# Kernel tuning notes

Measured on AMD Instinct MI355X. Metric: run time of the kernel, lower is better.

## Reference

```python
import jax, jax.numpy as jnp
import numpy as np

N_AGENTS = 5
RNN = 128
ATT = 64
N_ACT = 10
IN_DIM = 256
SIZE = 65535  # multiple of N_AGENTS -> padding branch never taken
TAU = 0.01


def _gru_cell(x, h, w_ih, w_hh, b_ih, b_hh):
    # PyTorch GRUCell math
    gi = x @ w_ih.T + b_ih
    gh = h @ w_hh.T + b_hh
    i_r, i_z, i_n = jnp.split(gi, 3, axis=-1)
    h_r, h_z, h_n = jnp.split(gh, 3, axis=-1)
    r = jax.nn.sigmoid(i_r + h_r)
    z = jax.nn.sigmoid(i_z + h_z)
    n = jnp.tanh(i_n + r * h_n)
    return (1.0 - z) * n + z * h


def _gru_seq(xs, w_ih, w_hh, b_ih, b_hh):
    # xs: [T, B, D]; zero initial hidden, returns all step outputs [T, B, RNN]
    h0 = jnp.zeros((xs.shape[1], RNN), xs.dtype)
    def step(h, x):
        h2 = _gru_cell(x, h, w_ih, w_hh, b_ih, b_hh)
        return h2, h2
    _, ys = jax.lax.scan(step, h0, xs)
    return ys


def setup_inputs():
    key = jax.random.key(0)
    ks = jax.random.split(key, 26)
    def u(k, shape, fan):
        return jax.random.uniform(k, shape, jnp.float32, -1.0, 1.0) / np.sqrt(fan)
    return {
        'obs': jax.random.normal(ks[0], (SIZE, IN_DIM), jnp.float32),
        'hidden_state': jax.random.normal(ks[1], (SIZE, RNN), jnp.float32),
        'enc_w': u(ks[2], (RNN, IN_DIM), IN_DIM), 'enc_b': u(ks[3], (RNN,), IN_DIM),
        'gru_w_ih': u(ks[4], (3 * RNN, RNN), RNN), 'gru_w_hh': u(ks[5], (3 * RNN, RNN), RNN),
        'gru_b_ih': u(ks[6], (3 * RNN,), RNN), 'gru_b_hh': u(ks[7], (3 * RNN,), RNN),
        'bi_w_ih_f': u(ks[8], (3 * RNN, 2 * RNN), RNN), 'bi_w_hh_f': u(ks[9], (3 * RNN, RNN), RNN),
        'bi_b_ih_f': u(ks[10], (3 * RNN,), RNN), 'bi_b_hh_f': u(ks[11], (3 * RNN,), RNN),
        'bi_w_ih_r': u(ks[12], (3 * RNN, 2 * RNN), RNN), 'bi_w_hh_r': u(ks[13], (3 * RNN, RNN), RNN),
        'bi_b_ih_r': u(ks[14], (3 * RNN,), RNN), 'bi_b_hh_r': u(ks[15], (3 * RNN,), RNN),
        'hard_w': u(ks[16], (2, 2 * RNN), 2 * RNN), 'hard_b': u(ks[17], (2,), 2 * RNN),
        'q_w': u(ks[18], (ATT, RNN), RNN),
        'k_w': u(ks[19], (ATT, RNN), RNN),
        'v_w': u(ks[20], (ATT, RNN), RNN), 'v_b': u(ks[21], (ATT,), RNN),
        'dec_w': u(ks[22], (N_ACT, RNN + ATT), RNN + ATT), 'dec_b': u(ks[23], (N_ACT,), RNN + ATT),
    }


def reference(obs, hidden_state, enc_w, enc_b, gru_w_ih, gru_w_hh, gru_b_ih, gru_b_hh,
              bi_w_ih_f, bi_w_hh_f, bi_b_ih_f, bi_b_hh_f,
              bi_w_ih_r, bi_w_hh_r, bi_b_ih_r, bi_b_hh_r,
              hard_w, hard_b, q_w, k_w, v_w, v_b, dec_w, dec_b):
    size = obs.shape[0]
    bpa = size // N_AGENTS  # batch per agent; SIZE is a multiple of N_AGENTS

    x = jax.nn.relu(obs @ enc_w.T + enc_b)
    h_out = _gru_cell(x, hidden_state, gru_w_ih, gru_w_hh, gru_b_ih, gru_b_hh)

    # --- hard attention: pairwise agent features -> bi-GRU -> gumbel-softmax gate ---
    # (computed exactly as in the original; note the original soft_attention
    #  ignores hard_weights, so this does not influence the returned output)
    h = h_out.reshape(bpa, N_AGENTS, RNN)
    nbr = np.array([[j for j in range(N_AGENTS) if j != i] for i in range(N_AGENTS)])  # [n, n-1]
    h_i = jnp.broadcast_to(h[:, :, None, :], (bpa, N_AGENTS, N_AGENTS - 1, RNN))
    h_j = h[:, nbr, :]                              # [bpa, n, n-1, RNN]
    pair = jnp.concatenate([h_i, h_j], axis=-1)     # [bpa, n, n-1, 2*RNN]
    seq = pair.transpose(2, 0, 1, 3).reshape(N_AGENTS - 1, bpa * N_AGENTS, 2 * RNN)
    fwd = _gru_seq(seq, bi_w_ih_f, bi_w_hh_f, bi_b_ih_f, bi_b_hh_f)
    bwd = _gru_seq(seq[::-1], bi_w_ih_r, bi_w_hh_r, bi_b_ih_r, bi_b_hh_r)[::-1]
    h_hard = jnp.concatenate([fwd, bwd], axis=-1)   # [n-1, B, 2*RNN]
    h_hard = h_hard.transpose(1, 0, 2).reshape(-1, 2 * RNN)
    logits = h_hard @ hard_w.T + hard_b             # [B*(n-1), 2]
    u01 = jax.random.uniform(jax.random.key(42), logits.shape, jnp.float32, 1e-10, 1.0)
    gumbel = -jnp.log(-jnp.log(u01))
    gs = jax.nn.softmax((logits + gumbel) / TAU, axis=-1)
    hard_weights = gs[:, 1].reshape(bpa, N_AGENTS, 1, N_AGENTS - 1).transpose(1, 0, 2, 3)
    _ = hard_weights  # unused downstream, matching the original module

    # --- soft attention: original loops per sample doing a 1x1 matmul+softmax;
    #     vectorized here. softmax over a single element is identically 1. ---
    q = h_out @ q_w.T
    k = h_out @ k_w.T
    v = jax.nn.relu(h_out @ v_w.T + v_b)
    score = jnp.sum(q * k, axis=-1, keepdims=True) / np.sqrt(ATT)  # [B,1]
    soft_w = jax.nn.softmax(score, axis=-1)                         # all ones
    x_att = v * soft_w

    final_input = jnp.concatenate([h_out, x_att], axis=-1)
    output = final_input @ dec_w.T + dec_b
    return output, h_out
```

## Files before the change

kernel.cpp:

```cpp
#include <hip/hip_runtime.h>
#include <stdint.h>

#define SIZE 65535

typedef __bf16 bf16x8 __attribute__((ext_vector_type(8)));
typedef float floatx4 __attribute__((ext_vector_type(4)));

#define WS_ENCW 0
#define WS_WIH  32768
#define WS_WHH  81920
#define WS_VW   131072
#define WS_DECW 139264
#define WS_TOTC 17792

__device__ __forceinline__ unsigned short f2bf(float f) {
    union { float f; unsigned int u; } v; v.f = f;
    unsigned int u = v.u;
    return (unsigned short)((u + 0x7fffu + ((u >> 16) & 1u)) >> 16);
}
__device__ __forceinline__ unsigned short f2bfn(float f) {
    union { __bf16 h; unsigned short s; } u; u.h = (__bf16)f;
    return u.s;
}
__device__ __forceinline__ float bf2f(unsigned short b) {
    union { unsigned int u; float f; } v; v.u = ((unsigned int)b) << 16;
    return v.f;
}
__device__ __forceinline__ float sigmf(float x) {
    x = fminf(fmaxf(x, -30.f), 30.f);
    return 1.f / (1.f + __expf(-x));
}
__device__ __forceinline__ float tanhfast(float x) {
    x = fminf(fmaxf(x, -15.f), 15.f);
    float e = __expf(2.f * x);
    return (e - 1.f) / (e + 1.f);
}

__device__ __forceinline__ bf16x8 cvt8g(const float* p) {
    float4 a = *reinterpret_cast<const float4*>(p);
    float4 b = *reinterpret_cast<const float4*>(p + 4);
    bf16x8 r;
    r[0] = (__bf16)a.x; r[1] = (__bf16)a.y; r[2] = (__bf16)a.z; r[3] = (__bf16)a.w;
    r[4] = (__bf16)b.x; r[5] = (__bf16)b.y; r[6] = (__bf16)b.z; r[7] = (__bf16)b.w;
    return r;
}
__device__ __forceinline__ bf16x8 ld8(const unsigned short* p) {
    return *reinterpret_cast<const bf16x8*>(p);
}

__device__ __forceinline__ void glds16(const unsigned short* g, unsigned short* l) {
    __builtin_amdgcn_global_load_lds(
        (const __attribute__((address_space(1))) unsigned int*)g,
        (__attribute__((address_space(3))) unsigned int*)l, 16, 0, 0);
}

__device__ __forceinline__ void stage_seq(unsigned short* dst, const unsigned short* src,
                                          int nfrags, int wave, int lane) {
    for (int s = wave; s < nfrags; s += 4)
        glds16(src + s * 512 + lane * 8, dst + s * 512);
}
__device__ __forceinline__ void stage_gru(unsigned short* dst, const unsigned short* wsw,
                                          int ng, int wave, int lane) {
    const int fo = (ng * 4 + wave) * 512 + lane * 8;
    glds16(wsw + WS_WIH + fo, dst + wave * 512);
    glds16(wsw + WS_WHH + fo, dst + (4 + wave) * 512);
}

__global__ __launch_bounds__(256) void cvt_weights(
    const float* __restrict__ enc_w, const float* __restrict__ w_ih,
    const float* __restrict__ w_hh, const float* __restrict__ v_w,
    const float* __restrict__ dec_w, unsigned short* __restrict__ ws) {
    int c = blockIdx.x * 256 + threadIdx.x;
    if (c >= WS_TOTC) return;
    const int lane = c & 63;
    const int l = lane & 15;
    const int q = lane >> 4;
    const float* src; int row, col, stride; bool zero = false;
    if (c < 4096) {
        int lt = c >> 6; int nt = lt >> 3, kt = lt & 7;
        row = nt * 16 + l; col = kt * 32 + q * 8; src = enc_w; stride = 256;
    } else if (c < 10240) {
        int lt = (c - 4096) >> 6; int nt = lt / 12; int r2 = lt % 12;
        int g = r2 >> 2, kt = r2 & 3;
        row = g * 128 + nt * 16 + l; col = kt * 32 + q * 8; src = w_ih; stride = 128;
    } else if (c < 16384) {
        int lt = (c - 10240) >> 6; int nt = lt / 12; int r2 = lt % 12;
        int g = r2 >> 2, kt = r2 & 3;
        row = g * 128 + nt * 16 + l; col = kt * 32 + q * 8; src = w_hh; stride = 128;
    } else if (c < 17408) {
        int lt = (c - 16384) >> 6; int nt = lt >> 2, kt = lt & 3;
        row = nt * 16 + l; col = kt * 32 + q * 8; src = v_w; stride = 128;
    } else {
        int kt = (c - 17408) >> 6;
        row = l; col = kt * 32 + q * 8; src = dec_w; stride = 192;
        zero = (l >= 10);
    }
    float4 a, b;
    if (zero) { a = make_float4(0.f,0.f,0.f,0.f); b = a; }
    else {
        const float* p = src + (size_t)row * stride + col;
        a = *reinterpret_cast<const float4*>(p);
        b = *reinterpret_cast<const float4*>(p + 4);
    }
    unsigned short* d = ws + (size_t)c * 8;
    d[0]=f2bf(a.x); d[1]=f2bf(a.y); d[2]=f2bf(a.z); d[3]=f2bf(a.w);
    d[4]=f2bf(b.x); d[5]=f2bf(b.y); d[6]=f2bf(b.z); d[7]=f2bf(b.w);
}

__global__ __launch_bounds__(256, 3) void attn_critic_kernel(
    const float* __restrict__ obs,
    const float* __restrict__ hid,
    const float* __restrict__ enc_b,
    const float* __restrict__ b_ih,
    const float* __restrict__ b_hh,
    const float* __restrict__ v_b,
    const float* __restrict__ dec_b,
    const unsigned short* __restrict__ wsw,
    float* __restrict__ out)
{
    __shared__ __align__(16) unsigned short wbuf[2][4096];
    __shared__ __align__(16) unsigned short pool[4][4352];

    const int tid  = threadIdx.x;
    const int wave = tid >> 6;
    const int lane = tid & 63;
    const int l15  = lane & 15;
    const int quad = lane >> 4;
    const int wrow0 = (blockIdx.x * 4 + wave) * 32;

    unsigned short (*sA)[136] = (unsigned short(*)[136])&pool[wave][0];
    unsigned short (*sV)[72]  = (unsigned short(*)[72]) &pool[wave][0];
    float* sO = (float*)&pool[wave][2304];

    int rA0 = wrow0 + l15;      rA0 = (rA0 < SIZE) ? rA0 : (SIZE - 1);
    int rA1 = wrow0 + 16 + l15; rA1 = (rA1 < SIZE) ? rA1 : (SIZE - 1);

    stage_seq(wbuf[0], wsw + WS_ENCW, 8, wave, lane);

    bf16x8 aob[2][8], hf[2][4];
    {
        const float* o0 = obs + (size_t)rA0 * 256;
        const float* o1 = obs + (size_t)rA1 * 256;
#pragma unroll
        for (int kt = 0; kt < 8; ++kt) {
            aob[0][kt] = cvt8g(o0 + kt * 32 + quad * 8);
            aob[1][kt] = cvt8g(o1 + kt * 32 + quad * 8);
        }
        const float* h0 = hid + (size_t)rA0 * 128;
        const float* h1 = hid + (size_t)rA1 * 128;
#pragma unroll
        for (int kt = 0; kt < 4; ++kt) {
            hf[0][kt] = cvt8g(h0 + kt * 32 + quad * 8);
            hf[1][kt] = cvt8g(h1 + kt * 32 + quad * 8);
        }
    }
    __builtin_amdgcn_sched_barrier(0);
    __syncthreads();

#pragma unroll 1
    for (int nt = 0; nt < 8; ++nt) {
        const int cur = nt & 1;
        if (nt < 7) stage_seq(wbuf[cur ^ 1], wsw + WS_ENCW + (nt + 1) * 4096, 8, wave, lane);
        else        stage_gru(wbuf[cur ^ 1], wsw, 0, wave, lane);
        const float bias = enc_b[nt * 16 + l15];
        floatx4 a0 = floatx4{0.f,0.f,0.f,0.f}, a1 = a0;
#pragma unroll
        for (int kt = 0; kt < 8; ++kt) {
            bf16x8 b = ld8(&wbuf[cur][kt * 512 + lane * 8]);
            a0 = __builtin_amdgcn_mfma_f32_16x16x32_bf16(aob[0][kt], b, a0, 0, 0, 0);
            a1 = __builtin_amdgcn_mfma_f32_16x16x32_bf16(aob[1][kt], b, a1, 0, 0, 0);
        }
#pragma unroll
        for (int r = 0; r < 4; ++r) {
            sA[quad * 4 + r][nt * 16 + l15]      = f2bfn(fmaxf(a0[r] + bias, 0.f));
            sA[16 + quad * 4 + r][nt * 16 + l15] = f2bfn(fmaxf(a1[r] + bias, 0.f));
        }
        __syncthreads();
    }

    bf16x8 xf[2][4];
#pragma unroll
    for (int kt = 0; kt < 4; ++kt) {
        xf[0][kt] = ld8(&sA[l15][kt * 32 + quad * 8]);
        xf[1][kt] = ld8(&sA[16 + l15][kt * 32 + quad * 8]);
    }

#pragma unroll 1
    for (int nt = 0; nt < 8; ++nt) {
        const int nr = nt * 16 + l15;
        float hp[2][4];
#pragma unroll
        for (int m = 0; m < 2; ++m)
#pragma unroll
            for (int r = 0; r < 4; ++r) {
                const int grow = wrow0 + m * 16 + quad * 4 + r;
                const int rowc = (grow < SIZE) ? grow : (SIZE - 1);
                hp[m][r] = hid[(size_t)rowc * 128 + nr];
            }
        const float bir_ = b_ih[nr], biz_ = b_ih[nr + 128], bin_ = b_ih[nr + 256];
        const float bhr_ = b_hh[nr], bhz_ = b_hh[nr + 128], bhn_ = b_hh[nr + 256];
        floatx4 gi[3][2], gh[3][2];
#pragma unroll
        for (int g = 0; g < 3; ++g) {
            gi[g][0] = floatx4{0.f,0.f,0.f,0.f}; gi[g][1] = gi[g][0];
            gh[g][0] = gi[g][0]; gh[g][1] = gi[g][0];
        }
#pragma unroll
        for (int g = 0; g < 3; ++g) {
            const int cur = (nt + g) & 1;
            const int ng = nt * 3 + g + 1;
            if (ng < 24) stage_gru(wbuf[cur ^ 1], wsw, ng, wave, lane);
            else         stage_seq(wbuf[cur ^ 1], wsw + WS_VW, 4, wave, lane);
#pragma unroll
            for (int kt = 0; kt < 4; ++kt) {
                bf16x8 bi = ld8(&wbuf[cur][kt * 512 + lane * 8]);
                bf16x8 bh = ld8(&wbuf[cur][(4 + kt) * 512 + lane * 8]);
                gi[g][0] = __builtin_amdgcn_mfma_f32_16x16x32_bf16(xf[0][kt], bi, gi[g][0], 0, 0, 0);
                gi[g][1] = __builtin_amdgcn_mfma_f32_16x16x32_bf16(xf[1][kt], bi, gi[g][1], 0, 0, 0);
                gh[g][0] = __builtin_amdgcn_mfma_f32_16x16x32_bf16(hf[0][kt], bh, gh[g][0], 0, 0, 0);
                gh[g][1] = __builtin_amdgcn_mfma_f32_16x16x32_bf16(hf[1][kt], bh, gh[g][1], 0, 0, 0);
            }
            __syncthreads();
        }
#pragma unroll
        for (int m = 0; m < 2; ++m)
#pragma unroll
            for (int r = 0; r < 4; ++r) {
                float rg = sigmf(gi[0][m][r] + bir_ + gh[0][m][r] + bhr_);
                float zg = sigmf(gi[1][m][r] + biz_ + gh[1][m][r] + bhz_);
                float ng2 = tanhfast(gi[2][m][r] + bin_ + rg * (gh[2][m][r] + bhn_));
                float ho = (1.f - zg) * ng2 + zg * hp[m][r];
                sA[m * 16 + quad * 4 + r][nr] = f2bfn(ho);
            }
    }

    bf16x8 af[2][4];
#pragma unroll
    for (int kt = 0; kt < 4; ++kt) {
        af[0][kt] = ld8(&sA[l15][kt * 32 + quad * 8]);
        af[1][kt] = ld8(&sA[16 + l15][kt * 32 + quad * 8]);
    }
    {
        float* out_h = out + (size_t)SIZE * 10;
#pragma unroll 1
        for (int it = 0; it < 16; ++it) {
            int idx = it * 256 + lane * 4;
            int rr = idx >> 7, cc = idx & 127;
            int grow = wrow0 + rr;
            if (grow < SIZE) {
                float2 p0 = make_float2(bf2f(sA[rr][cc]),     bf2f(sA[rr][cc + 1]));
                float2 p1 = make_float2(bf2f(sA[rr][cc + 2]), bf2f(sA[rr][cc + 3]));
                float* dst = out_h + (size_t)grow * 128 + cc;
                *reinterpret_cast<float2*>(dst)     = p0;
                *reinterpret_cast<float2*>(dst + 2) = p1;
            }
        }
    }

#pragma unroll 1
    for (int nt = 0; nt < 4; ++nt) {
        const int cur = nt & 1;
        if (nt < 3) stage_seq(wbuf[cur ^ 1], wsw + WS_VW + (nt + 1) * 2048, 4, wave, lane);
        else        stage_seq(wbuf[cur ^ 1], wsw + WS_DECW, 6, wave, lane);
        const float bias = v_b[nt * 16 + l15];
        floatx4 a0 = floatx4{0.f,0.f,0.f,0.f}, a1 = a0;
#pragma unroll
        for (int kt = 0; kt < 4; ++kt) {
            bf16x8 b = ld8(&wbuf[cur][kt * 512 + lane * 8]);
            a0 = __builtin_amdgcn_mfma_f32_16x16x32_bf16(af[0][kt], b, a0, 0, 0, 0);
            a1 = __builtin_amdgcn_mfma_f32_16x16x32_bf16(af[1][kt], b, a1, 0, 0, 0);
        }
#pragma unroll
        for (int r = 0; r < 4; ++r) {
            sV[quad * 4 + r][nt * 16 + l15]      = f2bfn(fmaxf(a0[r] + bias, 0.f));
            sV[16 + quad * 4 + r][nt * 16 + l15] = f2bfn(fmaxf(a1[r] + bias, 0.f));
        }
        __syncthreads();
    }

    {
        floatx4 d0 = floatx4{0.f,0.f,0.f,0.f}, d1 = d0;
#pragma unroll
        for (int kt = 0; kt < 6; ++kt) {
            bf16x8 b = ld8(&wbuf[0][kt * 512 + lane * 8]);
            bf16x8 a0 = (kt < 4) ? af[0][kt] : ld8(&sV[l15][(kt - 4) * 32 + quad * 8]);
            bf16x8 a1 = (kt < 4) ? af[1][kt] : ld8(&sV[16 + l15][(kt - 4) * 32 + quad * 8]);
            d0 = __builtin_amdgcn_mfma_f32_16x16x32_bf16(a0, b, d0, 0, 0, 0);
            d1 = __builtin_amdgcn_mfma_f32_16x16x32_bf16(a1, b, d1, 0, 0, 0);
        }
        if (l15 < 10) {
            const float bias = dec_b[l15];
#pragma unroll
            for (int r = 0; r < 4; ++r) {
                sO[(quad * 4 + r) * 10 + l15]      = d0[r] + bias;
                sO[(16 + quad * 4 + r) * 10 + l15] = d1[r] + bias;
            }
        }
#pragma unroll
        for (int j = 0; j < 5; ++j) {
            int idx = j * 64 + lane;
            int row = idx / 10, col = idx % 10;
            int grow = wrow0 + row;
            if (grow < SIZE)
                out[(size_t)grow * 10 + col] = sO[row * 10 + col];
        }
    }
}

extern "C" void kernel_launch(void* const* d_in, const int* in_sizes, int n_in,
                              void* d_out, int out_size, void* d_ws, size_t ws_size,
                              hipStream_t stream) {
    const float* obs   = (const float*)d_in[0];
    const float* hid   = (const float*)d_in[1];
    const float* enc_w = (const float*)d_in[2];
    const float* enc_b = (const float*)d_in[3];
    const float* w_ih  = (const float*)d_in[4];
    const float* w_hh  = (const float*)d_in[5];
    const float* b_ih  = (const float*)d_in[6];
    const float* b_hh  = (const float*)d_in[7];
    const float* v_w   = (const float*)d_in[20];
    const float* v_b   = (const float*)d_in[21];
    const float* dec_w = (const float*)d_in[22];
    const float* dec_b = (const float*)d_in[23];
    unsigned short* wsw = (unsigned short*)d_ws;
    float* out = (float*)d_out;

    hipLaunchKernelGGL(cvt_weights, dim3((WS_TOTC + 255) / 256), dim3(256), 0, stream,
                       enc_w, w_ih, w_hh, v_w, dec_w, wsw);
    hipLaunchKernelGGL(attn_critic_kernel, dim3(512), dim3(256), 0, stream,
                       obs, hid, enc_b, b_ih, b_hh, v_b, dec_b, wsw, out);
}
```

Measured before the change: 219.4 us.

## Double weight staging chunk size to halve block barriers across encoder, GRU, value stages

```diff
diff --git a/kernel.cpp b/kernel.cpp
--- a/kernel.cpp
+++ b/kernel.cpp
@@ -18,10 +18,6 @@
     unsigned int u = v.u;
     return (unsigned short)((u + 0x7fffu + ((u >> 16) & 1u)) >> 16);
 }
-__device__ __forceinline__ unsigned short f2bfn(float f) {
-    union { __bf16 h; unsigned short s; } u; u.h = (__bf16)f;
-    return u.s;
-}
 __device__ __forceinline__ float bf2f(unsigned short b) {
     union { unsigned int u; float f; } v; v.u = ((unsigned int)b) << 16;
     return v.f;
@@ -36,13 +32,15 @@
     return (e - 1.f) / (e + 1.f);
 }
 
+union BF8 { bf16x8 v; unsigned short s[8]; };
+
 __device__ __forceinline__ bf16x8 cvt8g(const float* p) {
     float4 a = *reinterpret_cast<const float4*>(p);
     float4 b = *reinterpret_cast<const float4*>(p + 4);
-    bf16x8 r;
-    r[0] = (__bf16)a.x; r[1] = (__bf16)a.y; r[2] = (__bf16)a.z; r[3] = (__bf16)a.w;
-    r[4] = (__bf16)b.x; r[5] = (__bf16)b.y; r[6] = (__bf16)b.z; r[7] = (__bf16)b.w;
-    return r;
+    BF8 r;
+    r.s[0] = f2bf(a.x); r.s[1] = f2bf(a.y); r.s[2] = f2bf(a.z); r.s[3] = f2bf(a.w);
+    r.s[4] = f2bf(b.x); r.s[5] = f2bf(b.y); r.s[6] = f2bf(b.z); r.s[7] = f2bf(b.w);
+    return r.v;
 }
 __device__ __forceinline__ bf16x8 ld8(const unsigned short* p) {
     return *reinterpret_cast<const bf16x8*>(p);
@@ -64,6 +62,11 @@
     const int fo = (ng * 4 + wave) * 512 + lane * 8;
     glds16(wsw + WS_WIH + fo, dst + wave * 512);
     glds16(wsw + WS_WHH + fo, dst + (4 + wave) * 512);
+}
+__device__ __forceinline__ void stage_gru2(unsigned short* dst, const unsigned short* wsw,
+                                           int ng0, int wave, int lane) {
+    stage_gru(dst, wsw, ng0, wave, lane);
+    stage_gru(dst + 4096, wsw, ng0 + 1, wave, lane);
 }
 
 __global__ __launch_bounds__(256) void cvt_weights(
@@ -107,7 +110,20 @@
     d[4]=f2bf(b.x); d[5]=f2bf(b.y); d[6]=f2bf(b.z); d[7]=f2bf(b.w);
 }
 
-__global__ __launch_bounds__(256, 3) void attn_critic_kernel(
+#define DO_NG(WB, G, GI, GH)                                                               \
+    {                                                                                      \
+        _Pragma("unroll")                                                                  \
+        for (int kt = 0; kt < 4; ++kt) {                                                   \
+            bf16x8 bi = ld8((WB) + kt * 512 + lane * 8);                                   \
+            bf16x8 bh = ld8((WB) + (4 + kt) * 512 + lane * 8);                             \
+            GI[G][0] = __builtin_amdgcn_mfma_f32_16x16x32_bf16(xf[0][kt], bi, GI[G][0], 0, 0, 0); \
+            GI[G][1] = __builtin_amdgcn_mfma_f32_16x16x32_bf16(xf[1][kt], bi, GI[G][1], 0, 0, 0); \
+            GH[G][0] = __builtin_amdgcn_mfma_f32_16x16x32_bf16(hf[0][kt], bh, GH[G][0], 0, 0, 0); \
+            GH[G][1] = __builtin_amdgcn_mfma_f32_16x16x32_bf16(hf[1][kt], bh, GH[G][1], 0, 0, 0); \
+        }                                                                                  \
+    }
+
+__global__ __launch_bounds__(256, 2) void attn_critic_kernel(
     const float* __restrict__ obs,
     const float* __restrict__ hid,
     const float* __restrict__ enc_b,
@@ -118,7 +134,7 @@
     const unsigned short* __restrict__ wsw,
     float* __restrict__ out)
 {
-    __shared__ __align__(16) unsigned short wbuf[2][4096];
+    __shared__ __align__(16) unsigned short wbuf[2][8192];
     __shared__ __align__(16) unsigned short pool[4][4352];
 
     const int tid  = threadIdx.x;
@@ -135,7 +151,7 @@
     int rA0 = wrow0 + l15;      rA0 = (rA0 < SIZE) ? rA0 : (SIZE - 1);
     int rA1 = wrow0 + 16 + l15; rA1 = (rA1 < SIZE) ? rA1 : (SIZE - 1);
 
-    stage_seq(wbuf[0], wsw + WS_ENCW, 8, wave, lane);
+    stage_seq(wbuf[0], wsw + WS_ENCW, 16, wave, lane);
 
     bf16x8 aob[2][8], hf[2][4];
     {
@@ -158,22 +174,27 @@
     __syncthreads();
 
 #pragma unroll 1
-    for (int nt = 0; nt < 8; ++nt) {
-        const int cur = nt & 1;
-        if (nt < 7) stage_seq(wbuf[cur ^ 1], wsw + WS_ENCW + (nt + 1) * 4096, 8, wave, lane);
-        else        stage_gru(wbuf[cur ^ 1], wsw, 0, wave, lane);
-        const float bias = enc_b[nt * 16 + l15];
-        floatx4 a0 = floatx4{0.f,0.f,0.f,0.f}, a1 = a0;
-#pragma unroll
-        for (int kt = 0; kt < 8; ++kt) {
-            bf16x8 b = ld8(&wbuf[cur][kt * 512 + lane * 8]);
-            a0 = __builtin_amdgcn_mfma_f32_16x16x32_bf16(aob[0][kt], b, a0, 0, 0, 0);
-            a1 = __builtin_amdgcn_mfma_f32_16x16x32_bf16(aob[1][kt], b, a1, 0, 0, 0);
-        }
-#pragma unroll
-        for (int r = 0; r < 4; ++r) {
-            sA[quad * 4 + r][nt * 16 + l15]      = f2bfn(fmaxf(a0[r] + bias, 0.f));
-            sA[16 + quad * 4 + r][nt * 16 + l15] = f2bfn(fmaxf(a1[r] + bias, 0.f));
+    for (int step = 0; step < 4; ++step) {
+        const int cur = step & 1;
+        if (step < 3) stage_seq(wbuf[cur ^ 1], wsw + WS_ENCW + (step + 1) * 8192, 16, wave, lane);
+        else          stage_gru2(wbuf[cur ^ 1], wsw, 0, wave, lane);
+#pragma unroll
+        for (int h = 0; h < 2; ++h) {
+            const int nt = step * 2 + h;
+            const unsigned short* wb = &wbuf[cur][h * 4096];
+            const float bias = enc_b[nt * 16 + l15];
+            floatx4 a0 = floatx4{0.f,0.f,0.f,0.f}, a1 = a0;
+#pragma unroll
+            for (int kt = 0; kt < 8; ++kt) {
+                bf16x8 b = ld8(wb + kt * 512 + lane * 8);
+                a0 = __builtin_amdgcn_mfma_f32_16x16x32_bf16(aob[0][kt], b, a0, 0, 0, 0);
+                a1 = __builtin_amdgcn_mfma_f32_16x16x32_bf16(aob[1][kt], b, a1, 0, 0, 0);
+            }
+#pragma unroll
+            for (int r = 0; r < 4; ++r) {
+                sA[quad * 4 + r][nt * 16 + l15]      = f2bf(fmaxf(a0[r] + bias, 0.f));
+                sA[16 + quad * 4 + r][nt * 16 + l15] = f2bf(fmaxf(a1[r] + bias, 0.f));
+            }
         }
         __syncthreads();
     }
@@ -186,52 +207,74 @@
     }
 
 #pragma unroll 1
-    for (int nt = 0; nt < 8; ++nt) {
-        const int nr = nt * 16 + l15;
-        float hp[2][4];
+    for (int u = 0; u < 4; ++u) {
+        const int nt0 = u * 2, nt1 = nt0 + 1;
+        const int nr0 = nt0 * 16 + l15, nr1 = nt1 * 16 + l15;
+        float hp0[2][4], hp1[2][4];
 #pragma unroll
         for (int m = 0; m < 2; ++m)
 #pragma unroll
             for (int r = 0; r < 4; ++r) {
                 const int grow = wrow0 + m * 16 + quad * 4 + r;
                 const int rowc = (grow < SIZE) ? grow : (SIZE - 1);
-                hp[m][r] = hid[(size_t)rowc * 128 + nr];
-            }
-        const float bir_ = b_ih[nr], biz_ = b_ih[nr + 128], bin_ = b_ih[nr + 256];
-        const float bhr_ = b_hh[nr], bhz_ = b_hh[nr + 128], bhn_ = b_hh[nr + 256];
-        floatx4 gi[3][2], gh[3][2];
+                hp0[m][r] = hid[(size_t)rowc * 128 + nr0];
+                hp1[m][r] = hid[(size_t)rowc * 128 + nr1];
+            }
+        const float bir0 = b_ih[nr0], biz0 = b_ih[nr0 + 128], bin0 = b_ih[nr0 + 256];
+        const float bhr0 = b_hh[nr0], bhz0 = b_hh[nr0 + 128], bhn0 = b_hh[nr0 + 256];
+        const float bir1 = b_ih[nr1], biz1 = b_ih[nr1 + 128], bin1 = b_ih[nr1 + 256];
+        const float bhr1 = b_hh[nr1], bhz1 = b_hh[nr1 + 128], bhn1 = b_hh[nr1 + 256];
+
+        floatx4 gi0[3][2], gh0[3][2], gi1[3][2], gh1[3][2];
 #pragma unroll
         for (int g = 0; g < 3; ++g) {
-            gi[g][0] = floatx4{0.f,0.f,0.f,0.f}; gi[g][1] = gi[g][0];
-            gh[g][0] = gi[g][0]; gh[g][1] = gi[g][0];
-        }
-#pragma unroll
-        for (int g = 0; g < 3; ++g) {
-            const int cur = (nt + g) & 1;
-            const int ng = nt * 3 + g + 1;
-            if (ng < 24) stage_gru(wbuf[cur ^ 1], wsw, ng, wave, lane);
-            else         stage_seq(wbuf[cur ^ 1], wsw + WS_VW, 4, wave, lane);
-#pragma unroll
-            for (int kt = 0; kt < 4; ++kt) {
-                bf16x8 bi = ld8(&wbuf[cur][kt * 512 + lane * 8]);
-                bf16x8 bh = ld8(&wbuf[cur][(4 + kt) * 512 + lane * 8]);
-                gi[g][0] = __builtin_amdgcn_mfma_f32_16x16x32_bf16(xf[0][kt], bi, gi[g][0], 0, 0, 0);
-                gi[g][1] = __builtin_amdgcn_mfma_f32_16x16x32_bf16(xf[1][kt], bi, gi[g][1], 0, 0, 0);
-                gh[g][0] = __builtin_amdgcn_mfma_f32_16x16x32_bf16(hf[0][kt], bh, gh[g][0], 0, 0, 0);
-                gh[g][1] = __builtin_amdgcn_mfma_f32_16x16x32_bf16(hf[1][kt], bh, gh[g][1], 0, 0, 0);
-            }
+            gi0[g][0] = floatx4{0.f,0.f,0.f,0.f}; gi0[g][1] = gi0[g][0];
+            gh0[g][0] = gi0[g][0]; gh0[g][1] = gi0[g][0];
+            gi1[g][0] = gi0[g][0]; gi1[g][1] = gi0[g][0];
+            gh1[g][0] = gi0[g][0]; gh1[g][1] = gi0[g][0];
+        }
+        {
+            const int cur = u & 1;
+            stage_gru2(wbuf[cur ^ 1], wsw, 6 * u + 2, wave, lane);
+            DO_NG(&wbuf[cur][0],    0, gi0, gh0);
+            DO_NG(&wbuf[cur][4096], 1, gi0, gh0);
             __syncthreads();
         }
-#pragma unroll
-        for (int m = 0; m < 2; ++m)
-#pragma unroll
-            for (int r = 0; r < 4; ++r) {
-                float rg = sigmf(gi[0][m][r] + bir_ + gh[0][m][r] + bhr_);
-                float zg = sigmf(gi[1][m][r] + biz_ + gh[1][m][r] + bhz_);
-                float ng2 = tanhfast(gi[2][m][r] + bin_ + rg * (gh[2][m][r] + bhn_));
-                float ho = (1.f - zg) * ng2 + zg * hp[m][r];
-                sA[m * 16 + quad * 4 + r][nr] = f2bfn(ho);
-            }
+        {
+            const int cur = (u + 1) & 1;
+            stage_gru2(wbuf[cur ^ 1], wsw, 6 * u + 4, wave, lane);
+            DO_NG(&wbuf[cur][0],    2, gi0, gh0);
+            DO_NG(&wbuf[cur][4096], 0, gi1, gh1);
+            __syncthreads();
+#pragma unroll
+            for (int m = 0; m < 2; ++m)
+#pragma unroll
+                for (int r = 0; r < 4; ++r) {
+                    float rg = sigmf(gi0[0][m][r] + bir0 + gh0[0][m][r] + bhr0);
+                    float zg = sigmf(gi0[1][m][r] + biz0 + gh0[1][m][r] + bhz0);
+                    float ng2 = tanhfast(gi0[2][m][r] + bin0 + rg * (gh0[2][m][r] + bhn0));
+                    float ho = (1.f - zg) * ng2 + zg * hp0[m][r];
+                    sA[m * 16 + quad * 4 + r][nr0] = f2bf(ho);
+                }
+        }
+        {
+            const int cur = u & 1;
+            if (u < 3) stage_gru2(wbuf[cur ^ 1], wsw, 6 * u + 6, wave, lane);
+            else       stage_seq(wbuf[cur ^ 1], wsw + WS_VW, 16, wave, lane);
+            DO_NG(&wbuf[cur][0],    1, gi1, gh1);
+            DO_NG(&wbuf[cur][4096], 2, gi1, gh1);
+            __syncthreads();
+#pragma unroll
+            for (int m = 0; m < 2; ++m)
+#pragma unroll
+                for (int r = 0; r < 4; ++r) {
+                    float rg = sigmf(gi1[0][m][r] + bir1 + gh1[0][m][r] + bhr1);
+                    float zg = sigmf(gi1[1][m][r] + biz1 + gh1[1][m][r] + bhz1);
+                    float ng2 = tanhfast(gi1[2][m][r] + bin1 + rg * (gh1[2][m][r] + bhn1));
+                    float ho = (1.f - zg) * ng2 + zg * hp1[m][r];
+                    sA[m * 16 + quad * 4 + r][nr1] = f2bf(ho);
+                }
+        }
     }
 
     bf16x8 af[2][4];
@@ -257,32 +300,30 @@
         }
     }
 
+    stage_seq(wbuf[1], wsw + WS_DECW, 6, wave, lane);
 #pragma unroll 1
     for (int nt = 0; nt < 4; ++nt) {
-        const int cur = nt & 1;
-        if (nt < 3) stage_seq(wbuf[cur ^ 1], wsw + WS_VW + (nt + 1) * 2048, 4, wave, lane);
-        else        stage_seq(wbuf[cur ^ 1], wsw + WS_DECW, 6, wave, lane);
         const float bias = v_b[nt * 16 + l15];
         floatx4 a0 = floatx4{0.f,0.f,0.f,0.f}, a1 = a0;
 #pragma unroll
         for (int kt = 0; kt < 4; ++kt) {
-            bf16x8 b = ld8(&wbuf[cur][kt * 512 + lane * 8]);
+            bf16x8 b = ld8(&wbuf[0][(nt * 4 + kt) * 512 + lane * 8]);
             a0 = __builtin_amdgcn_mfma_f32_16x16x32_bf16(af[0][kt], b, a0, 0, 0, 0);
             a1 = __builtin_amdgcn_mfma_f32_16x16x32_bf16(af[1][kt], b, a1, 0, 0, 0);
         }
 #pragma unroll
         for (int r = 0; r < 4; ++r) {
-            sV[quad * 4 + r][nt * 16 + l15]      = f2bfn(fmaxf(a0[r] + bias, 0.f));
-            sV[16 + quad * 4 + r][nt * 16 + l15] = f2bfn(fmaxf(a1[r] + bias, 0.f));
-        }
-        __syncthreads();
-    }
+            sV[quad * 4 + r][nt * 16 + l15]      = f2bf(fmaxf(a0[r] + bias, 0.f));
+            sV[16 + quad * 4 + r][nt * 16 + l15] = f2bf(fmaxf(a1[r] + bias, 0.f));
+        }
+    }
+    __syncthreads();
 
     {
         floatx4 d0 = floatx4{0.f,0.f,0.f,0.f}, d1 = d0;
 #pragma unroll
         for (int kt = 0; kt < 6; ++kt) {
-            bf16x8 b = ld8(&wbuf[0][kt * 512 + lane * 8]);
+            bf16x8 b = ld8(&wbuf[1][kt * 512 + lane * 8]);
             bf16x8 a0 = (kt < 4) ? af[0][kt] : ld8(&sV[l15][(kt - 4) * 32 + quad * 8]);
             bf16x8 a1 = (kt < 4) ? af[1][kt] : ld8(&sV[16 + l15][(kt - 4) * 32 + quad * 8]);
             d0 = __builtin_amdgcn_mfma_f32_16x16x32_bf16(a0, b, d0, 0, 0, 0);
```

After: 211.4 us. 3.7% less time.
